# Kernel optimization log

Measured on AMD Instinct MI355X. Metric: run time of the kernel, lower is better.

## Reference

```python
import jax, jax.numpy as jnp
import numpy as np

STATE_DIM, SKILL_DIM = 256, 64
HID = 1024
LAT = 128
B = 4096
TEMP = 1.0


def _init_linear(key, fan_in, fan_out):
    # torch nn.Linear default init: U(-1/sqrt(fan_in), 1/sqrt(fan_in))
    kw, kb = jax.random.split(key)
    bound = 1.0 / np.sqrt(fan_in)
    W = jax.random.uniform(kw, (fan_in, fan_out), jnp.float32, -bound, bound)
    b = jax.random.uniform(kb, (fan_out,), jnp.float32, -bound, bound)
    return W, b


def setup_inputs() -> dict:
    key = jax.random.key(0)
    ks = jax.random.split(key, 8)
    x = jax.random.normal(ks[0], (B, STATE_DIM), jnp.float32)
    y = jax.random.normal(ks[1], (B, SKILL_DIM), jnp.float32)
    sW1, sb1 = _init_linear(ks[2], STATE_DIM, HID)
    sW2, sb2 = _init_linear(ks[3], HID, HID)
    sW3, sb3 = _init_linear(ks[4], HID, LAT)
    kW1, kb1 = _init_linear(ks[5], SKILL_DIM, HID)
    kW2, kb2 = _init_linear(ks[6], HID, HID)
    kW3, kb3 = _init_linear(ks[7], HID, LAT)
    return {
        "x": x, "y": y,
        "sW1": sW1, "sb1": sb1, "sW2": sW2, "sb2": sb2, "sW3": sW3, "sb3": sb3,
        "kW1": kW1, "kb1": kb1, "kW2": kW2, "kb2": kb2, "kW3": kW3, "kb3": kb3,
    }


def _mlp(x, W1, b1, W2, b2, W3, b3):
    h = jax.nn.relu(x @ W1 + b1)
    h = jax.nn.relu(h @ W2 + b2)
    return h @ W3 + b3


def _l2norm(v, eps=1e-12):
    # matches F.normalize(dim=-1): v / max(||v||, eps)
    n = jnp.sqrt(jnp.sum(v * v, axis=-1, keepdims=True))
    return v / jnp.maximum(n, eps)


def reference(x, y, sW1, sb1, sW2, sb2, sW3, sb3, kW1, kb1, kW2, kb2, kW3, kb3):
    zx = _l2norm(_mlp(x, sW1, sb1, sW2, sb2, sW3, sb3))  # [B, LAT]
    zy = _l2norm(_mlp(y, kW1, kb1, kW2, kb2, kW3, kb3))  # [B, LAT]
    # sum(x[:,None,:]*y[None,:,:], -1) == zx @ zy.T (same math, no BxBxD blowup)
    scores = jnp.einsum('id,jd->ij', zx, zy) / TEMP       # [B, B]
    # InfoNCE lower bound: log(B) - CE(scores, arange(B)), reduction='none'
    logp = jax.nn.log_softmax(scores, axis=-1)
    nll = jnp.diagonal(logp)                               # = -CE per row
    mi = jnp.log(jnp.float32(scores.shape[0])) + nll       # [B]
    return scores, mi
```

## Files before the change

kernel.cpp:

```cpp
#include <hip/hip_runtime.h>
#include <hip/hip_bf16.h>
#include <math.h>

typedef __bf16 v8bf __attribute__((ext_vector_type(8)));
typedef float  v4f  __attribute__((ext_vector_type(4)));

#define GPTR(p) ((const __attribute__((address_space(1))) void*)(p))
#define LPTR(p) ((__attribute__((address_space(3))) void*)(p))

template <int N> __device__ __forceinline__ void waitvm() {
    if constexpr (N == 0) asm volatile("s_waitcnt vmcnt(0)" ::: "memory");
    else if constexpr (N == 5) asm volatile("s_waitcnt vmcnt(5)" ::: "memory");
    else asm volatile("s_waitcnt vmcnt(8)" ::: "memory");
}
#define WAITLGKM() asm volatile("s_waitcnt lgkmcnt(0)" ::: "memory")
#define BAR() __builtin_amdgcn_s_barrier()
#define SCHEDBAR() __builtin_amdgcn_sched_barrier(0)

struct PrepArgs {
    const float* x; const float* y;
    __hip_bfloat16* xb; __hip_bfloat16* yb;
    int nx4, ntot4;
    const float* wsrc[6];
    __hip_bfloat16* wdst[6];
    int K[6], N[6];
};

__global__ __launch_bounds__(256)
void prep_k(PrepArgs a) {
    const int tid = threadIdx.x, bx = blockIdx.x, z = blockIdx.z;
    if (z == 0) {
        int i = bx * 256 + tid;
        if (i >= a.ntot4) return;
        const float* src; __hip_bfloat16* dst; int j;
        if (i < a.nx4) { src = a.x; dst = a.xb; j = i; }
        else           { src = a.y; dst = a.yb; j = i - a.nx4; }
        float4 v = ((const float4*)src)[j];
        __hip_bfloat16 h[4] = {__float2bfloat16(v.x), __float2bfloat16(v.y),
                               __float2bfloat16(v.z), __float2bfloat16(v.w)};
        ((short4*)dst)[j] = *(short4*)h;
        return;
    }
    int w = z - 1;
    int K = a.K[w], N = a.N[w];
    int tn = N >> 5;
    int tt = (K >> 5) * tn;
    if (bx >= tt) return;
    int kt = (bx / tn) * 32, nt = (bx % tn) * 32;
    __shared__ float t[32][33];
    int tx = tid & 31, ty = tid >> 5;
    const float* W = a.wsrc[w];
    __hip_bfloat16* Wt = a.wdst[w];
#pragma unroll
    for (int i = 0; i < 4; ++i)
        t[ty + i * 8][tx] = W[(size_t)(kt + ty + i * 8) * N + nt + tx];
    __syncthreads();
#pragma unroll
    for (int i = 0; i < 4; ++i)
        Wt[(size_t)(nt + ty + i * 8) * K + kt + tx] =
            __float2bfloat16(t[tx][ty + i * 8]);
}

__device__ __forceinline__ void stage128(
    const __hip_bfloat16* __restrict__ A, const __hip_bfloat16* __restrict__ Bt,
    int lda, int ldb, int bm, int bn, int k0, int wid, int crow, int ccol,
    __hip_bfloat16* As, __hip_bfloat16* Bs) {
#pragma unroll
    for (int i = 0; i < 4; ++i) {
        int c = wid * 4 + i;
        __builtin_amdgcn_global_load_lds(
            GPTR(A + (size_t)(bm + c * 8 + crow) * lda + k0 + ccol),
            LPTR(As + c * 512), 16, 0, 0);
        __builtin_amdgcn_global_load_lds(
            GPTR(Bt + (size_t)(bn + c * 8 + crow) * ldb + k0 + ccol),
            LPTR(Bs + c * 512), 16, 0, 0);
    }
}

__device__ __forceinline__ void compute128(
    const __hip_bfloat16* As, const __hip_bfloat16* Bs,
    int lane, int wr, int wc, v4f acc[4][4]) {
#pragma unroll
    for (int kk = 0; kk < 64; kk += 32) {
        v8bf a[4], b[4];
#pragma unroll
        for (int i = 0; i < 4; ++i) {
            a[i] = *(const v8bf*)&As[(wr * 64 + i * 16 + (lane & 15)) * 64 + kk + (lane >> 4) * 8];
            b[i] = *(const v8bf*)&Bs[(wc * 64 + i * 16 + (lane & 15)) * 64 + kk + (lane >> 4) * 8];
        }
#pragma unroll
        for (int i = 0; i < 4; ++i)
#pragma unroll
            for (int j = 0; j < 4; ++j)
                acc[i][j] = __builtin_amdgcn_mfma_f32_16x16x32_bf16(
                    a[i], b[j], acc[i][j], 0, 0, 0);
    }
}

struct MlpArgs {
    const __hip_bfloat16* A[2];
    const __hip_bfloat16* B[2];
    const float* bias[2];
    __hip_bfloat16* C[2];
    int K[2];
};

__global__ __launch_bounds__(256)
void gemm_mlp_k(MlpArgs args) {
    __shared__ __align__(16) __hip_bfloat16 As[2][128 * 64], Bs[2][128 * 64];
    const int bid = blockIdx.x;
    const int wg  = (bid & 7) * 64 + (bid >> 3);
    const int z   = wg >> 8;
    const int rem = wg & 255;
    const int bm  = (rem >> 3) * 128;
    const int bn  = (rem & 7) * 128;

    const int tid = threadIdx.x, wid = tid >> 6, lane = tid & 63;
    const int wr = wid >> 1, wc = wid & 1;
    const int crow = lane >> 3, ccol = (lane & 7) * 8;
    const __hip_bfloat16* A  = args.A[z];
    const __hip_bfloat16* Bt = args.B[z];
    const int K = args.K[z];
    const int nt = K >> 6;

    v4f acc[4][4] = {};
    stage128(A, Bt, K, K, bm, bn, 0, wid, crow, ccol, As[0], Bs[0]);
    int cur = 0;
    for (int t = 0; t < nt - 1; ++t) {
        stage128(A, Bt, K, K, bm, bn, (t + 1) * 64, wid, crow, ccol,
                 As[cur ^ 1], Bs[cur ^ 1]);
        waitvm<8>(); BAR(); SCHEDBAR();
        compute128(As[cur], Bs[cur], lane, wr, wc, acc);
        WAITLGKM(); BAR();
        cur ^= 1;
    }
    waitvm<0>(); BAR(); SCHEDBAR();
    compute128(As[cur], Bs[cur], lane, wr, wc, acc);

    const float* bias = args.bias[z];
    __hip_bfloat16* C = args.C[z];
#pragma unroll
    for (int i = 0; i < 4; ++i) {
        int rowb = bm + wr * 64 + i * 16 + (lane >> 4) * 4;
#pragma unroll
        for (int j = 0; j < 4; ++j) {
            int col = bn + wc * 64 + j * 16 + (lane & 15);
            float bv = bias[col];
#pragma unroll
            for (int r = 0; r < 4; ++r) {
                float v = fmaxf(acc[i][j][r] + bv, 0.f);
                C[(size_t)(rowb + r) * 1024 + col] = __float2bfloat16(v);
            }
        }
    }
}

__global__ __launch_bounds__(256)
void gemm_l3norm_k(const __hip_bfloat16* __restrict__ As_g0,
                   const __hip_bfloat16* __restrict__ As_g1,
                   const __hip_bfloat16* __restrict__ Bt0,
                   const __hip_bfloat16* __restrict__ Bt1,
                   const float* __restrict__ sb3, const float* __restrict__ kb3,
                   __hip_bfloat16* __restrict__ zxb,
                   __hip_bfloat16* __restrict__ zyb) {
    __shared__ __align__(16) __hip_bfloat16 As[2][32 * 64];
    __shared__ __align__(16) __hip_bfloat16 Bs[2][128 * 64];
    __shared__ float red[4][32];
    const int bid = blockIdx.x;
    const int wg  = (bid & 7) * 32 + (bid >> 3);
    const int z   = wg >> 7;
    const int bm  = (wg & 127) * 32;

    const __hip_bfloat16* A  = z ? As_g1 : As_g0;
    const __hip_bfloat16* Bt = z ? Bt1 : Bt0;
    const float* bias = z ? kb3 : sb3;
    __hip_bfloat16* zout = z ? zyb : zxb;

    const int tid = threadIdx.x, wid = tid >> 6, lane = tid & 63;
    const int crow = lane >> 3, ccol = (lane & 7) * 8;

    auto stage = [&](int buf, int k0) {
        __builtin_amdgcn_global_load_lds(
            GPTR(A + (size_t)(bm + wid * 8 + crow) * 1024 + k0 + ccol),
            LPTR(&As[buf][wid * 512]), 16, 0, 0);
#pragma unroll
        for (int i = 0; i < 4; ++i) {
            int c = wid * 4 + i;
            __builtin_amdgcn_global_load_lds(
                GPTR(Bt + (size_t)(c * 8 + crow) * 1024 + k0 + ccol),
                LPTR(&Bs[buf][c * 512]), 16, 0, 0);
        }
    };
    auto compute = [&](int buf, v4f acc[2][2]) {
#pragma unroll
        for (int kk = 0; kk < 64; kk += 32) {
            v8bf a[2], b[2];
#pragma unroll
            for (int i = 0; i < 2; ++i)
                a[i] = *(const v8bf*)&As[buf][(i * 16 + (lane & 15)) * 64 + kk + (lane >> 4) * 8];
#pragma unroll
            for (int j = 0; j < 2; ++j)
                b[j] = *(const v8bf*)&Bs[buf][(wid * 32 + j * 16 + (lane & 15)) * 64 + kk + (lane >> 4) * 8];
#pragma unroll
            for (int i = 0; i < 2; ++i)
#pragma unroll
                for (int j = 0; j < 2; ++j)
                    acc[i][j] = __builtin_amdgcn_mfma_f32_16x16x32_bf16(
                        a[i], b[j], acc[i][j], 0, 0, 0);
        }
    };

    v4f acc[2][2] = {};
    stage(0, 0);
    int cur = 0;
    for (int t = 0; t < 15; ++t) {
        stage(cur ^ 1, (t + 1) * 64);
        waitvm<5>(); BAR(); SCHEDBAR();
        compute(cur, acc);
        WAITLGKM(); BAR();
        cur ^= 1;
    }
    waitvm<0>(); BAR(); SCHEDBAR();
    compute(cur, acc);

    float val[2][2][4];
    float ssq[2][4];
#pragma unroll
    for (int i = 0; i < 2; ++i)
#pragma unroll
        for (int r = 0; r < 4; ++r) ssq[i][r] = 0.f;
#pragma unroll
    for (int i = 0; i < 2; ++i)
#pragma unroll
        for (int j = 0; j < 2; ++j) {
            int col = wid * 32 + j * 16 + (lane & 15);
            float bv = bias[col];
#pragma unroll
            for (int r = 0; r < 4; ++r) {
                float v = acc[i][j][r] + bv;
                val[i][j][r] = v;
                ssq[i][r] += v * v;
            }
        }
#pragma unroll
    for (int i = 0; i < 2; ++i)
#pragma unroll
        for (int r = 0; r < 4; ++r) {
#pragma unroll
            for (int m = 1; m < 16; m <<= 1)
                ssq[i][r] += __shfl_xor(ssq[i][r], m, 64);
            if ((lane & 15) == 0)
                red[wid][i * 16 + (lane >> 4) * 4 + r] = ssq[i][r];
        }
    __syncthreads();
#pragma unroll
    for (int i = 0; i < 2; ++i)
#pragma unroll
        for (int r = 0; r < 4; ++r) {
            int row = i * 16 + (lane >> 4) * 4 + r;
            float ss = red[0][row] + red[1][row] + red[2][row] + red[3][row];
            float inv = 1.0f / fmaxf(sqrtf(ss), 1e-12f);
#pragma unroll
            for (int j = 0; j < 2; ++j) {
                int col = wid * 32 + j * 16 + (lane & 15);
                zout[(size_t)(bm + row) * 128 + col] =
                    __float2bfloat16(val[i][j][r] * inv);
            }
        }
}

__global__ __launch_bounds__(256)
void gemm_scores_k(const __hip_bfloat16* __restrict__ zxb,
                   const __hip_bfloat16* __restrict__ zyb,
                   float* __restrict__ out, float* __restrict__ esum) {
    __shared__ __align__(16) __hip_bfloat16 As[128 * 64], Bs[128 * 64];
    __shared__ float rowsum[2][128];
    const int tid = threadIdx.x, wid = tid >> 6, lane = tid & 63;
    const int wr = wid >> 1, wc = wid & 1;
    const int bm = blockIdx.x * 128, bn = blockIdx.y * 128;
    const int crow = lane >> 3, ccol = (lane & 7) * 8;
    v4f acc[4][4] = {};
#pragma unroll
    for (int t = 0; t < 2; ++t) {
        stage128(zxb, zyb, 128, 128, bm, bn, t * 64, wid, crow, ccol, As, Bs);
        __syncthreads();
        compute128(As, Bs, lane, wr, wc, acc);
        __syncthreads();
    }
#pragma unroll
    for (int i = 0; i < 4; ++i) {
        int rowb = bm + wr * 64 + i * 16 + (lane >> 4) * 4;
#pragma unroll
        for (int r = 0; r < 4; ++r) {
            float s = 0.f;
#pragma unroll
            for (int j = 0; j < 4; ++j) {
                int col = bn + wc * 64 + j * 16 + (lane & 15);
                float v = acc[i][j][r];
                __builtin_nontemporal_store(v, &out[(size_t)(rowb + r) * 4096 + col]);
                s += __expf(v - 1.0f);
            }
#pragma unroll
            for (int m = 1; m < 16; m <<= 1) s += __shfl_xor(s, m, 64);
            if ((lane & 15) == 0)
                rowsum[wc][wr * 64 + i * 16 + (lane >> 4) * 4 + r] = s;
        }
    }
    __syncthreads();
    if (tid < 128)
        esum[(size_t)(bm + tid) * 32 + blockIdx.y] =
            rowsum[0][tid] + rowsum[1][tid];
}

__global__ __launch_bounds__(256)
void mi_k(const float* __restrict__ esum, const float* __restrict__ scores,
          float* __restrict__ mi) {
    int row = blockIdx.x * 256 + threadIdx.x;
    const float4* p = (const float4*)&esum[(size_t)row * 32];
    float s = 0.f;
#pragma unroll
    for (int i = 0; i < 8; ++i) { float4 v = p[i]; s += v.x + v.y + v.z + v.w; }
    float diag = scores[(size_t)row * 4096 + row];
    mi[row] = 8.317766166719343f + diag - 1.0f - logf(s);
}

extern "C" void kernel_launch(void* const* d_in, const int* in_sizes, int n_in,
                              void* d_out, int out_size, void* d_ws, size_t ws_size,
                              hipStream_t stream) {
    const float* x   = (const float*)d_in[0];
    const float* y   = (const float*)d_in[1];
    const float* sW1 = (const float*)d_in[2];
    const float* sb1 = (const float*)d_in[3];
    const float* sW2 = (const float*)d_in[4];
    const float* sb2 = (const float*)d_in[5];
    const float* sW3 = (const float*)d_in[6];
    const float* sb3 = (const float*)d_in[7];
    const float* kW1 = (const float*)d_in[8];
    const float* kb1 = (const float*)d_in[9];
    const float* kW2 = (const float*)d_in[10];
    const float* kb2 = (const float*)d_in[11];
    const float* kW3 = (const float*)d_in[12];
    const float* kb3 = (const float*)d_in[13];

    float* out = (float*)d_out;
    float* mi  = out + (size_t)4096 * 4096;

    char* ws = (char*)d_ws;
    auto alloc = [&](size_t bytes) {
        char* p = ws;
        ws += (bytes + 255) & ~(size_t)255;
        return p;
    };
    __hip_bfloat16* xb   = (__hip_bfloat16*)alloc((size_t)4096 * 256 * 2);
    __hip_bfloat16* yb   = (__hip_bfloat16*)alloc((size_t)4096 * 64 * 2);
    __hip_bfloat16* sW1t = (__hip_bfloat16*)alloc((size_t)1024 * 256 * 2);
    __hip_bfloat16* sW2t = (__hip_bfloat16*)alloc((size_t)1024 * 1024 * 2);
    __hip_bfloat16* sW3t = (__hip_bfloat16*)alloc((size_t)128 * 1024 * 2);
    __hip_bfloat16* kW1t = (__hip_bfloat16*)alloc((size_t)1024 * 64 * 2);
    __hip_bfloat16* kW2t = (__hip_bfloat16*)alloc((size_t)1024 * 1024 * 2);
    __hip_bfloat16* kW3t = (__hip_bfloat16*)alloc((size_t)128 * 1024 * 2);
    __hip_bfloat16* h1s  = (__hip_bfloat16*)alloc((size_t)4096 * 1024 * 2);
    __hip_bfloat16* h1k  = (__hip_bfloat16*)alloc((size_t)4096 * 1024 * 2);
    __hip_bfloat16* h2s  = (__hip_bfloat16*)alloc((size_t)4096 * 1024 * 2);
    __hip_bfloat16* h2k  = (__hip_bfloat16*)alloc((size_t)4096 * 1024 * 2);
    float*          es   = (float*)alloc((size_t)4096 * 32 * 4);
    __hip_bfloat16* zxb  = (__hip_bfloat16*)alloc((size_t)4096 * 128 * 2);
    __hip_bfloat16* zyb  = (__hip_bfloat16*)alloc((size_t)4096 * 128 * 2);

    PrepArgs pa;
    pa.x = x; pa.y = y; pa.xb = xb; pa.yb = yb;
    pa.nx4 = 4096 * 256 / 4;
    pa.ntot4 = pa.nx4 + 4096 * 64 / 4;
    pa.wsrc[0] = sW1; pa.wdst[0] = sW1t; pa.K[0] = 256;  pa.N[0] = 1024;
    pa.wsrc[1] = sW2; pa.wdst[1] = sW2t; pa.K[1] = 1024; pa.N[1] = 1024;
    pa.wsrc[2] = sW3; pa.wdst[2] = sW3t; pa.K[2] = 1024; pa.N[2] = 128;
    pa.wsrc[3] = kW1; pa.wdst[3] = kW1t; pa.K[3] = 64;   pa.N[3] = 1024;
    pa.wsrc[4] = kW2; pa.wdst[4] = kW2t; pa.K[4] = 1024; pa.N[4] = 1024;
    pa.wsrc[5] = kW3; pa.wdst[5] = kW3t; pa.K[5] = 1024; pa.N[5] = 128;
    prep_k<<<dim3(1280, 1, 7), 256, 0, stream>>>(pa);

    MlpArgs l1;
    l1.A[0] = xb;  l1.B[0] = sW1t; l1.bias[0] = sb1; l1.C[0] = h1s; l1.K[0] = 256;
    l1.A[1] = yb;  l1.B[1] = kW1t; l1.bias[1] = kb1; l1.C[1] = h1k; l1.K[1] = 64;
    gemm_mlp_k<<<512, 256, 0, stream>>>(l1);

    MlpArgs l2;
    l2.A[0] = h1s; l2.B[0] = sW2t; l2.bias[0] = sb2; l2.C[0] = h2s; l2.K[0] = 1024;
    l2.A[1] = h1k; l2.B[1] = kW2t; l2.bias[1] = kb2; l2.C[1] = h2k; l2.K[1] = 1024;
    gemm_mlp_k<<<512, 256, 0, stream>>>(l2);

    gemm_l3norm_k<<<256, 256, 0, stream>>>(
        h2s, h2k, sW3t, kW3t, sb3, kb3, zxb, zyb);

    gemm_scores_k<<<dim3(32, 32), 256, 0, stream>>>(zxb, zyb, out, es);

    mi_k<<<16, 256, 0, stream>>>(es, out, mi);
}
```

Before: 90.40 us.

## Drop double-buffered LDS pipeline and stage MLP GEMM output through LDS

Replaces the double-buffered global-to-LDS prefetch loop in both GEMM kernels with a single-buffer load, sync, compute, sync loop. This frees LDS, possibly raising occupancy. The MLP GEMM epilogue now writes bias+ReLU results into a padded LDS tile and stores them to global memory as contiguous 16-byte vectors, so writes are coalesced. The cost is that memory loads no longer overlap with MFMA compute, and the epilogue adds extra barriers.

```diff
diff --git a/kernel.cpp b/kernel.cpp
--- a/kernel.cpp
+++ b/kernel.cpp
@@ -7,15 +7,6 @@
 
 #define GPTR(p) ((const __attribute__((address_space(1))) void*)(p))
 #define LPTR(p) ((__attribute__((address_space(3))) void*)(p))
-
-template <int N> __device__ __forceinline__ void waitvm() {
-    if constexpr (N == 0) asm volatile("s_waitcnt vmcnt(0)" ::: "memory");
-    else if constexpr (N == 5) asm volatile("s_waitcnt vmcnt(5)" ::: "memory");
-    else asm volatile("s_waitcnt vmcnt(8)" ::: "memory");
-}
-#define WAITLGKM() asm volatile("s_waitcnt lgkmcnt(0)" ::: "memory")
-#define BAR() __builtin_amdgcn_s_barrier()
-#define SCHEDBAR() __builtin_amdgcn_sched_barrier(0)
 
 struct PrepArgs {
     const float* x; const float* y;
@@ -107,7 +98,10 @@
 
 __global__ __launch_bounds__(256)
 void gemm_mlp_k(MlpArgs args) {
-    __shared__ __align__(16) __hip_bfloat16 As[2][128 * 64], Bs[2][128 * 64];
+    __shared__ __align__(16) __hip_bfloat16 As[128 * 64];
+    __shared__ __align__(16) __hip_bfloat16 Bs[128 * 64];
+    __shared__ __align__(16) __hip_bfloat16 Cs[64][136];
+
     const int bid = blockIdx.x;
     const int wg  = (bid & 7) * 64 + (bid >> 3);
     const int z   = wg >> 8;
@@ -121,37 +115,42 @@
     const __hip_bfloat16* A  = args.A[z];
     const __hip_bfloat16* Bt = args.B[z];
     const int K = args.K[z];
-    const int nt = K >> 6;
 
     v4f acc[4][4] = {};
-    stage128(A, Bt, K, K, bm, bn, 0, wid, crow, ccol, As[0], Bs[0]);
-    int cur = 0;
-    for (int t = 0; t < nt - 1; ++t) {
-        stage128(A, Bt, K, K, bm, bn, (t + 1) * 64, wid, crow, ccol,
-                 As[cur ^ 1], Bs[cur ^ 1]);
-        waitvm<8>(); BAR(); SCHEDBAR();
-        compute128(As[cur], Bs[cur], lane, wr, wc, acc);
-        WAITLGKM(); BAR();
-        cur ^= 1;
-    }
-    waitvm<0>(); BAR(); SCHEDBAR();
-    compute128(As[cur], Bs[cur], lane, wr, wc, acc);
+    for (int k0 = 0; k0 < K; k0 += 64) {
+        stage128(A, Bt, K, K, bm, bn, k0, wid, crow, ccol, As, Bs);
+        __syncthreads();
+        compute128(As, Bs, lane, wr, wc, acc);
+        __syncthreads();
+    }
 
     const float* bias = args.bias[z];
     __hip_bfloat16* C = args.C[z];
 #pragma unroll
-    for (int i = 0; i < 4; ++i) {
-        int rowb = bm + wr * 64 + i * 16 + (lane >> 4) * 4;
-#pragma unroll
-        for (int j = 0; j < 4; ++j) {
-            int col = bn + wc * 64 + j * 16 + (lane & 15);
-            float bv = bias[col];
-#pragma unroll
-            for (int r = 0; r < 4; ++r) {
-                float v = fmaxf(acc[i][j][r] + bv, 0.f);
-                C[(size_t)(rowb + r) * 1024 + col] = __float2bfloat16(v);
-            }
-        }
+    for (int p = 0; p < 2; ++p) {
+        if (wr == p) {
+#pragma unroll
+            for (int i = 0; i < 4; ++i)
+#pragma unroll
+                for (int j = 0; j < 4; ++j) {
+                    float bv = bias[bn + wc * 64 + j * 16 + (lane & 15)];
+#pragma unroll
+                    for (int r = 0; r < 4; ++r) {
+                        float v = fmaxf(acc[i][j][r] + bv, 0.f);
+                        Cs[i * 16 + (lane >> 4) * 4 + r]
+                          [wc * 64 + j * 16 + (lane & 15)] = __float2bfloat16(v);
+                    }
+                }
+        }
+        __syncthreads();
+        int row = tid >> 2, q = tid & 3;
+        size_t gb = (size_t)(bm + p * 64 + row) * 1024 + bn + q * 32;
+#pragma unroll
+        for (int k = 0; k < 4; ++k) {
+            v8bf t = *(const v8bf*)&Cs[row][q * 32 + k * 8];
+            *(v8bf*)&C[gb + k * 8] = t;
+        }
+        __syncthreads();
     }
 }
 
@@ -163,8 +162,8 @@
                    const float* __restrict__ sb3, const float* __restrict__ kb3,
                    __hip_bfloat16* __restrict__ zxb,
                    __hip_bfloat16* __restrict__ zyb) {
-    __shared__ __align__(16) __hip_bfloat16 As[2][32 * 64];
-    __shared__ __align__(16) __hip_bfloat16 Bs[2][128 * 64];
+    __shared__ __align__(16) __hip_bfloat16 As[32 * 64];
+    __shared__ __align__(16) __hip_bfloat16 Bs[128 * 64];
     __shared__ float red[4][32];
     const int bid = blockIdx.x;
     const int wg  = (bid & 7) * 32 + (bid >> 3);
@@ -179,28 +178,28 @@
     const int tid = threadIdx.x, wid = tid >> 6, lane = tid & 63;
     const int crow = lane >> 3, ccol = (lane & 7) * 8;
 
-    auto stage = [&](int buf, int k0) {
+    v4f acc[2][2] = {};
+    for (int k0 = 0; k0 < 1024; k0 += 64) {
         __builtin_amdgcn_global_load_lds(
             GPTR(A + (size_t)(bm + wid * 8 + crow) * 1024 + k0 + ccol),
-            LPTR(&As[buf][wid * 512]), 16, 0, 0);
+            LPTR(&As[wid * 512]), 16, 0, 0);
 #pragma unroll
         for (int i = 0; i < 4; ++i) {
             int c = wid * 4 + i;
             __builtin_amdgcn_global_load_lds(
                 GPTR(Bt + (size_t)(c * 8 + crow) * 1024 + k0 + ccol),
-                LPTR(&Bs[buf][c * 512]), 16, 0, 0);
-        }
-    };
-    auto compute = [&](int buf, v4f acc[2][2]) {
+                LPTR(&Bs[c * 512]), 16, 0, 0);
+        }
+        __syncthreads();
 #pragma unroll
         for (int kk = 0; kk < 64; kk += 32) {
             v8bf a[2], b[2];
 #pragma unroll
             for (int i = 0; i < 2; ++i)
-                a[i] = *(const v8bf*)&As[buf][(i * 16 + (lane & 15)) * 64 + kk + (lane >> 4) * 8];
+                a[i] = *(const v8bf*)&As[(i * 16 + (lane & 15)) * 64 + kk + (lane >> 4) * 8];
 #pragma unroll
             for (int j = 0; j < 2; ++j)
-                b[j] = *(const v8bf*)&Bs[buf][(wid * 32 + j * 16 + (lane & 15)) * 64 + kk + (lane >> 4) * 8];
+                b[j] = *(const v8bf*)&Bs[(wid * 32 + j * 16 + (lane & 15)) * 64 + kk + (lane >> 4) * 8];
 #pragma unroll
             for (int i = 0; i < 2; ++i)
 #pragma unroll
@@ -208,20 +207,8 @@
                     acc[i][j] = __builtin_amdgcn_mfma_f32_16x16x32_bf16(
                         a[i], b[j], acc[i][j], 0, 0, 0);
         }
-    };
-
-    v4f acc[2][2] = {};
-    stage(0, 0);
-    int cur = 0;
-    for (int t = 0; t < 15; ++t) {
-        stage(cur ^ 1, (t + 1) * 64);
-        waitvm<5>(); BAR(); SCHEDBAR();
-        compute(cur, acc);
-        WAITLGKM(); BAR();
-        cur ^= 1;
-    }
-    waitvm<0>(); BAR(); SCHEDBAR();
-    compute(cur, acc);
+        __syncthreads();
+    }
 
     float val[2][2][4];
     float ssq[2][4];
```

Result: slower. 98.66 us (+9.1%).
